# Performance work log

Measured on AMD Instinct MI355X. Metric: run time of the kernel, lower is better.

The kernel has to match this reference:

```python
import jax, jax.numpy as jnp
import numpy as np

B, L, V, D, C, R = 8, 2048, 32000, 512, 64, 64
NBLK = 2           # n_layers - 1
H = 2 * D          # stem hidden dim
STD = 0.02


def _ln(x, w, b):
    m = x.mean(-1, keepdims=True)
    v = ((x - m) ** 2).mean(-1, keepdims=True)
    return (x - m) / jnp.sqrt(v + 1e-5) * w + b


def setup_inputs() -> dict:
    key = jax.random.key(0)
    ks = jax.random.split(key, 16)
    n = lambda k, shp: jax.random.normal(k, shp, dtype=jnp.float32) * STD
    return {
        "token_ids": jax.random.randint(ks[0], (B, L), 0, V),
        "tok_emb": n(ks[1], (V, D)),
        "pos_emb": n(ks[2], (L, D)),
        "stem_ln_w": jnp.ones((NBLK, D), jnp.float32),
        "stem_ln_b": jnp.zeros((NBLK, D), jnp.float32),
        "stem_w1": n(ks[3], (NBLK, D, H)),
        "stem_b1": jnp.zeros((NBLK, H), jnp.float32),
        "stem_w2": n(ks[4], (NBLK, H, D)),
        "stem_b2": jnp.zeros((NBLK, D), jnp.float32),
        "role_ln_w": jnp.ones((D,), jnp.float32),
        "role_ln_b": jnp.zeros((D,), jnp.float32),
        "Wa": n(ks[5], (D, R)),
        "Wb": n(ks[6], (D, R)),
        "Wc": n(ks[7], (D, R)),
        "class_a": n(ks[8], (C, R)),
        "class_b": n(ks[9], (C, R)),
        "class_c": n(ks[10], (C, R)),
        "query_ln_w": jnp.ones((D,), jnp.float32),
        "query_ln_b": jnp.zeros((D,), jnp.float32),
        "Wq": n(ks[11], (D, C)),
        "bq": jnp.zeros((C,), jnp.float32),
    }


def reference(token_ids, tok_emb, pos_emb, stem_ln_w, stem_ln_b, stem_w1,
              stem_b1, stem_w2, stem_b2, role_ln_w, role_ln_b, Wa, Wb, Wc,
              class_a, class_b, class_c, query_ln_w, query_ln_b, Wq, bq):
    seq_len = token_ids.shape[1]
    x = tok_emb[token_ids] + pos_emb[:seq_len][None, :, :]  # [B,L,D]
    for i in range(NBLK):
        h = _ln(x, stem_ln_w[i], stem_ln_b[i])
        h = jax.nn.gelu(h @ stem_w1[i] + stem_b1[i], approximate=False)
        x = x + h @ stem_w2[i] + stem_b2[i]
    prefix = _ln(x[:, :-1], role_ln_w, role_ln_b)  # [B,L-1,D]
    a = jnp.tanh(prefix @ Wa)
    b = jnp.tanh(prefix @ Wb)
    c = jnp.tanh(prefix @ Wc)
    ua = jnp.einsum('blr,cr->blc', a, class_a)  # [B,L-1,C]
    ub = jnp.einsum('blr,cr->blc', b, class_b)
    uc = jnp.einsum('blr,cr->blc', c, class_c)
    # exact ordered-triplet sum  sum_{i<j<k} ua_i * ub_j * uc_k  via exclusive cumsums
    prefA = jnp.cumsum(ua, axis=1) - ua            # sum_{i<j} ua_i
    t = ub * prefA
    prefT = jnp.cumsum(t, axis=1) - t              # sum_{j<k} ub_j * prefA_j
    s = (uc * prefT).sum(axis=1)                   # [B,C]
    Lp = max(seq_len - 1, 1)
    denom = max(Lp * (Lp - 1) * (Lp - 2) / 6.0, 1.0)
    q = _ln(x[:, -1], query_ln_w, query_ln_b)
    return s / denom + q @ Wq + bq
```

## Files before the change

kernel.cpp:

```cpp
#include <hip/hip_runtime.h>

#define NROWS 16384
#define LSEQ  2048
#define NB    8

typedef short v8s __attribute__((ext_vector_type(8)));
typedef float v4f __attribute__((ext_vector_type(4)));

__device__ __forceinline__ unsigned short f2bf(float f) {
    unsigned int u = __float_as_uint(f);
    return (unsigned short)((u + 0x7fffu + ((u >> 16) & 1u)) >> 16);
}
__device__ __forceinline__ float bf2f(unsigned short u) {
    return __uint_as_float(((unsigned int)u) << 16);
}

__device__ __forceinline__ void glds16(const void* g, void* l) {
    __builtin_amdgcn_global_load_lds(
        (__attribute__((address_space(1))) void*)g,
        (__attribute__((address_space(3))) void*)l,
        16, 0, 0);
}

__device__ __forceinline__ float fast_gelu(float v) {
    float z = fabsf(v) * 0.70710678118654752f;
    float t = __builtin_amdgcn_rcpf(1.0f + 0.3275911f * z);
    float poly = t * (0.254829592f + t * (-0.284496736f + t * (1.421413741f +
                 t * (-1.453152027f + t * 1.061405429f))));
    float erfz = 1.0f - poly * __expf(-z * z);
    float er = copysignf(erfz, v);
    return 0.5f * v * (1.0f + er);
}
__device__ __forceinline__ float fast_tanh(float y) {
    float e = __expf(2.0f * y);
    return (e - 1.0f) * __builtin_amdgcn_rcpf(e + 1.0f);
}

__device__ __forceinline__ long swizzled_row(int b, int wave) {
    int T = (b & 7) + (((b >> 3) & 15) << 3);
    int chunk = b >> 7;
    return (long)T * 128 + chunk * 4 + wave;
}

__global__ __launch_bounds__(256) void setup_kernel(
        const int* __restrict__ ids,
        const float* __restrict__ tok, const float* __restrict__ pos,
        const float* __restrict__ g0, const float* __restrict__ b0,
        unsigned short* __restrict__ x, unsigned short* __restrict__ hl,
        const float* __restrict__ w1, const float* __restrict__ w2,
        const float* __restrict__ wa, const float* __restrict__ wb, const float* __restrict__ wc,
        const float* __restrict__ ca, const float* __restrict__ cb, const float* __restrict__ cc,
        unsigned short* __restrict__ w1T, unsigned short* __restrict__ w2T,
        unsigned short* __restrict__ wabcT, unsigned short* __restrict__ clsb) {
    int blk = blockIdx.x;
    int t = threadIdx.x;
    if (blk < 4096) {
        int wave = t >> 6, lane = t & 63;
        long row = swizzled_row(blk, wave);
        int l = (int)(row & (LSEQ - 1));
        int id = ids[row];
        int d = lane * 8;
        float4 t0 = *(const float4*)(tok + (size_t)id * 512 + d);
        float4 t1 = *(const float4*)(tok + (size_t)id * 512 + d + 4);
        float4 p0 = *(const float4*)(pos + (size_t)l * 512 + d);
        float4 p1 = *(const float4*)(pos + (size_t)l * 512 + d + 4);
        float a[8] = {t0.x + p0.x, t0.y + p0.y, t0.z + p0.z, t0.w + p0.w,
                      t1.x + p1.x, t1.y + p1.y, t1.z + p1.z, t1.w + p1.w};
        unsigned int xp[4];
        #pragma unroll
        for (int i = 0; i < 4; ++i)
            xp[i] = (unsigned int)f2bf(a[2 * i]) | ((unsigned int)f2bf(a[2 * i + 1]) << 16);
        *(uint4*)(x + row * 512 + d) = *(uint4*)xp;
        float s = 0.f, s2 = 0.f;
        #pragma unroll
        for (int i = 0; i < 8; ++i) { s += a[i]; s2 += a[i] * a[i]; }
        #pragma unroll
        for (int o = 32; o > 0; o >>= 1) { s += __shfl_down(s, o); s2 += __shfl_down(s2, o); }
        s = __shfl(s, 0); s2 = __shfl(s2, 0);
        float m = s * (1.0f / 512.0f);
        float rinv = 1.0f / sqrtf(s2 * (1.0f / 512.0f) - m * m + 1e-5f);
        float4 ga = *(const float4*)(g0 + d), gb = *(const float4*)(g0 + d + 4);
        float4 ba = *(const float4*)(b0 + d), bb2 = *(const float4*)(b0 + d + 4);
        float gg[8] = {ga.x, ga.y, ga.z, ga.w, gb.x, gb.y, gb.z, gb.w};
        float bb[8] = {ba.x, ba.y, ba.z, ba.w, bb2.x, bb2.y, bb2.z, bb2.w};
        unsigned int hp[4];
        #pragma unroll
        for (int i = 0; i < 4; ++i) {
            unsigned short lo = f2bf((a[2 * i]     - m) * rinv * gg[2 * i]     + bb[2 * i]);
            unsigned short hi = f2bf((a[2 * i + 1] - m) * rinv * gg[2 * i + 1] + bb[2 * i + 1]);
            hp[i] = (unsigned int)lo | ((unsigned int)hi << 16);
        }
        *(uint4*)(hl + row * 512 + d) = *(uint4*)hp;
    } else if (blk < 6240) {
        int id = blk - 4096;
        int tx = t & 31, ty = t >> 5;
        const float* in; unsigned short* out; int R, C, bx, by, ldo;
        if (id < 1024) {
            int l = id >> 9, r = id & 511;
            in = w1 + l * 524288; out = w1T + l * 524288;
            R = 512; C = 1024; bx = r & 31; by = r >> 5; ldo = 512;
        } else if (id < 2048) {
            int l = (id - 1024) >> 9, r = (id - 1024) & 511;
            in = w2 + l * 524288; out = w2T + l * 524288;
            R = 1024; C = 512; bx = r & 15; by = r >> 4; ldo = 1024;
        } else {
            int g = (id - 2048) >> 5, r = (id - 2048) & 31;
            in = (g == 0) ? wa : (g == 1) ? wb : wc;
            out = wabcT + g * 32768;
            R = 512; C = 64; bx = r & 1; by = r >> 1; ldo = 512;
        }
        __shared__ unsigned short tile[32][33];
        int c0 = bx * 32, r0 = by * 32;
        for (int i = ty; i < 32; i += 8) {
            int r = r0 + i, c = c0 + tx;
            tile[i][tx] = (r < R && c < C) ? f2bf(in[(size_t)r * C + c]) : (unsigned short)0;
        }
        __syncthreads();
        for (int i = ty; i < 32; i += 8) {
            int c = c0 + i, r = r0 + tx;
            if (r < R && c < C) out[(size_t)c * ldo + r] = tile[tx][i];
        }
    } else {
        int g = blk - 6240;
        const float* src = (g == 0) ? ca : (g == 1) ? cb : cc;
        unsigned short* dst = clsb + g * 4096;
        for (int i = t; i < 4096; i += 256) dst[i] = f2bf(src[i]);
    }
}

__global__ __launch_bounds__(256) void ln_kernel(const unsigned short* __restrict__ x,
        const float* __restrict__ g, const float* __restrict__ b,
        unsigned short* __restrict__ out) {
    int wave = threadIdx.x >> 6, lane = threadIdx.x & 63;
    long row = swizzled_row(blockIdx.x, wave);
    int d = lane * 8;
    uint4 xp = *(const uint4*)(x + row * 512 + d);
    const unsigned int* xw = (const unsigned int*)&xp;
    float a[8];
    #pragma unroll
    for (int i = 0; i < 4; ++i) {
        a[2 * i]     = bf2f((unsigned short)(xw[i] & 0xffff));
        a[2 * i + 1] = bf2f((unsigned short)(xw[i] >> 16));
    }
    float s = 0.f, s2 = 0.f;
    #pragma unroll
    for (int i = 0; i < 8; ++i) { s += a[i]; s2 += a[i] * a[i]; }
    #pragma unroll
    for (int o = 32; o > 0; o >>= 1) { s += __shfl_down(s, o); s2 += __shfl_down(s2, o); }
    s = __shfl(s, 0); s2 = __shfl(s2, 0);
    float m = s * (1.0f / 512.0f);
    float rinv = 1.0f / sqrtf(s2 * (1.0f / 512.0f) - m * m + 1e-5f);
    float4 g0 = *(const float4*)(g + d), g1 = *(const float4*)(g + d + 4);
    float4 b0 = *(const float4*)(b + d), b1 = *(const float4*)(b + d + 4);
    float gg[8] = {g0.x, g0.y, g0.z, g0.w, g1.x, g1.y, g1.z, g1.w};
    float bb[8] = {b0.x, b0.y, b0.z, b0.w, b1.x, b1.y, b1.z, b1.w};
    unsigned int hp[4];
    #pragma unroll
    for (int i = 0; i < 4; ++i) {
        unsigned short lo = f2bf((a[2 * i]     - m) * rinv * gg[2 * i]     + bb[2 * i]);
        unsigned short hi = f2bf((a[2 * i + 1] - m) * rinv * gg[2 * i + 1] + bb[2 * i + 1]);
        hp[i] = (unsigned int)lo | ((unsigned int)hi << 16);
    }
    *(uint4*)(out + row * 512 + d) = *(uint4*)hp;
}

#define EPI_GELU_BF16  0
#define EPI_RES_BF16   1

template <int EPI, int TN>
__global__ __launch_bounds__(256) void gemm_db(
        const unsigned short* __restrict__ A, int lda,
        const unsigned short* __restrict__ BT, int ldb,
        const float* __restrict__ bias,
        const unsigned short* __restrict__ xres,
        unsigned short* __restrict__ Cout, int ldc, int K) {
    constexpr int NJ = TN / 32;
    constexpr int BCH = TN / 64;
    constexpr int NL = 2 + BCH;
    __shared__ unsigned short As[3][128 * 32] __attribute__((aligned(16)));
    __shared__ unsigned short Bs[3][TN * 32] __attribute__((aligned(16)));
    const int t = threadIdx.x;
    const int lane = t & 63, wave = t >> 6;
    const int quad = lane >> 4, l16 = lane & 15;
    const int wm = (wave >> 1) * 64, wn = (wave & 1) * (TN / 2);
    const long tileM = (long)blockIdx.x * 128, tileN = (long)blockIdx.y * TN;

    const int lr = lane >> 2, lc = (lane & 3) * 8;
    const unsigned short* gA0 = A + (tileM + wave * 32 + lr) * (size_t)lda + lc;
    const unsigned short* gA1 = gA0 + 16 * (size_t)lda;
    const unsigned short* gB0 = BT + (tileN + wave * (BCH * 16) + lr) * (size_t)ldb + lc;
    const unsigned short* gB1 = gB0 + 16 * (size_t)ldb;

    v4f acc[4][NJ] = {};

    auto stage = [&](unsigned short* ab, unsigned short* bb) {
        glds16(gA0, ab + wave * 1024);
        glds16(gA1, ab + wave * 1024 + 512);
        glds16(gB0, bb + wave * (BCH * 512));
        if constexpr (BCH == 2) glds16(gB1, bb + wave * 1024 + 512);
        gA0 += 32; gA1 += 32; gB0 += 32;
        if constexpr (BCH == 2) gB1 += 32;
    };

    unsigned short *a0 = As[0], *a1 = As[1], *a2 = As[2];
    unsigned short *b0 = Bs[0], *b1 = Bs[1], *b2 = Bs[2];

    stage(a0, b0);
    stage(a1, b1);

    const int nk = K >> 5;
    for (int kk = 0; kk < nk; ++kk) {
        if (kk + 2 < nk) {
            stage(a2, b2);
            asm volatile("s_waitcnt vmcnt(%0)" :: "i"(2 * NL) : "memory");
        } else if (kk + 1 < nk) {
            asm volatile("s_waitcnt vmcnt(%0)" :: "i"(NL) : "memory");
        } else {
            asm volatile("s_waitcnt vmcnt(0)" ::: "memory");
        }
        asm volatile("s_barrier" ::: "memory");
        v8s af[4], bfr[NJ];
        #pragma unroll
        for (int i = 0; i < 4; ++i)
            af[i] = *(const v8s*)(a0 + (wm + i * 16 + l16) * 32 + quad * 8);
        #pragma unroll
        for (int j = 0; j < NJ; ++j)
            bfr[j] = *(const v8s*)(b0 + (wn + j * 16 + l16) * 32 + quad * 8);
        #pragma unroll
        for (int i = 0; i < 4; ++i)
            #pragma unroll
            for (int j = 0; j < NJ; ++j)
                acc[i][j] = __builtin_amdgcn_mfma_f32_16x16x32_bf16(bfr[j], af[i], acc[i][j], 0, 0, 0);
        if (kk + 1 < nk)
            asm volatile("s_barrier" ::: "memory");
        unsigned short* ta = a0; a0 = a1; a1 = a2; a2 = ta;
        unsigned short* tb = b0; b0 = b1; b1 = b2; b2 = tb;
    }

    #pragma unroll
    for (int i = 0; i < 4; ++i) {
        long m = tileM + wm + i * 16 + l16;
        #pragma unroll
        for (int j = 0; j < NJ; ++j) {
            long n0 = tileN + wn + j * 16 + quad * 4;
            float4 bi = *(const float4*)&bias[n0];
            const float* bip = (const float*)&bi;
            unsigned short pk[4];
            if (EPI == EPI_GELU_BF16) {
                #pragma unroll
                for (int r = 0; r < 4; ++r)
                    pk[r] = f2bf(fast_gelu(acc[i][j][r] + bip[r]));
            } else {
                ushort4 xr4 = *(const ushort4*)&xres[m * ldc + n0];
                const unsigned short* xp = (const unsigned short*)&xr4;
                #pragma unroll
                for (int r = 0; r < 4; ++r)
                    pk[r] = f2bf(acc[i][j][r] + bip[r] + bf2f(xp[r]));
            }
            *(ushort4*)&Cout[m * ldc + n0] = *(ushort4*)pk;
        }
    }
}

__global__ __launch_bounds__(256) void tanh_class_kernel(
        const unsigned short* __restrict__ A,
        const unsigned short* __restrict__ WT,
        const unsigned short* __restrict__ cls,
        unsigned short* __restrict__ uu) {
    __shared__ unsigned short As[128][40] __attribute__((aligned(16)));
    __shared__ unsigned short Bs[64][40] __attribute__((aligned(16)));
    __shared__ unsigned short P[128 * 72] __attribute__((aligned(16)));
    const int t = threadIdx.x;
    const int lane = t & 63, wave = t >> 6;
    const int quad = lane >> 4, l16 = lane & 15;
    const int wm = (wave >> 1) * 64, wn = (wave & 1) * 32;
    const long tileM = (long)blockIdx.x * 128;
    const int g = blockIdx.y;
    const int arow = t >> 2, acol = (t & 3) * 8;

    const unsigned short* BT = WT + g * 32768;
    v8s cf[2][2];
    #pragma unroll
    for (int ks = 0; ks < 2; ++ks)
        #pragma unroll
        for (int j = 0; j < 2; ++j)
            cf[ks][j] = *(const v8s*)&cls[g * 4096 + (wn + j * 16 + l16) * 64 + ks * 32 + quad * 8];

    const unsigned short* gA0 = A + (tileM + arow) * 512 + acol;
    const unsigned short* gA1 = gA0 + 64 * 512;
    const unsigned short* gB0 = BT + arow * 512 + acol;

    v4f acc[4][2] = {};
    uint4 a0, a1, b0;
    a0 = *(const uint4*)gA0; a1 = *(const uint4*)gA1; gA0 += 32; gA1 += 32;
    b0 = *(const uint4*)gB0; gB0 += 32;
    *(uint4*)&As[arow][acol] = a0;
    *(uint4*)&As[arow + 64][acol] = a1;
    *(uint4*)&Bs[arow][acol] = b0;

    for (int kk = 0; kk < 16; ++kk) {
        __syncthreads();
        const bool more = kk < 15;
        if (more) {
            a0 = *(const uint4*)gA0; a1 = *(const uint4*)gA1; gA0 += 32; gA1 += 32;
            b0 = *(const uint4*)gB0; gB0 += 32;
        }
        v8s af[4], bfr[2];
        #pragma unroll
        for (int i = 0; i < 4; ++i) af[i] = *(const v8s*)&As[wm + i * 16 + l16][quad * 8];
        #pragma unroll
        for (int j = 0; j < 2; ++j) bfr[j] = *(const v8s*)&Bs[wn + j * 16 + l16][quad * 8];
        #pragma unroll
        for (int i = 0; i < 4; ++i)
            #pragma unroll
            for (int j = 0; j < 2; ++j)
                acc[i][j] = __builtin_amdgcn_mfma_f32_16x16x32_bf16(bfr[j], af[i], acc[i][j], 0, 0, 0);
        __syncthreads();
        if (more) {
            *(uint4*)&As[arow][acol] = a0;
            *(uint4*)&As[arow + 64][acol] = a1;
            *(uint4*)&Bs[arow][acol] = b0;
        }
    }

    #pragma unroll
    for (int i = 0; i < 4; ++i) {
        int m = wm + i * 16 + l16;
        #pragma unroll
        for (int j = 0; j < 2; ++j) {
            int n0 = wn + j * 16 + quad * 4;
            unsigned short pk[4];
            #pragma unroll
            for (int r = 0; r < 4; ++r) pk[r] = f2bf(fast_tanh(acc[i][j][r]));
            *(ushort4*)&P[m * 72 + n0] = *(ushort4*)pk;
        }
    }
    __syncthreads();

    v4f acc2[4][2] = {};
    #pragma unroll
    for (int ks = 0; ks < 2; ++ks) {
        v8s paf[4];
        #pragma unroll
        for (int i = 0; i < 4; ++i)
            paf[i] = *(const v8s*)&P[(wm + i * 16 + l16) * 72 + ks * 32 + quad * 8];
        #pragma unroll
        for (int i = 0; i < 4; ++i)
            #pragma unroll
            for (int j = 0; j < 2; ++j)
                acc2[i][j] = __builtin_amdgcn_mfma_f32_16x16x32_bf16(cf[ks][j], paf[i], acc2[i][j], 0, 0, 0);
    }

    #pragma unroll
    for (int i = 0; i < 4; ++i) {
        long m = tileM + wm + i * 16 + l16;
        #pragma unroll
        for (int j = 0; j < 2; ++j) {
            int c0 = wn + j * 16 + quad * 4;
            unsigned short pk[4];
            #pragma unroll
            for (int r = 0; r < 4; ++r) pk[r] = f2bf(acc2[i][j][r]);
            *(ushort4*)&uu[m * 192 + g * 64 + c0] = *(ushort4*)pk;
        }
    }
}

__global__ __launch_bounds__(64) void scan_part_kernel(const unsigned short* __restrict__ u,
                                                       float* __restrict__ part) {
    int b = blockIdx.x, seg = blockIdx.y;
    int c = threadIdx.x;
    int l0 = seg * 32;
    int l1 = l0 + 32; if (l1 > 2047) l1 = 2047;
    float sA = 0.f, sB = 0.f, sC = 0.f, T = 0.f, M = 0.f, U = 0.f;
    const unsigned short* base = u + ((size_t)b * LSEQ + l0) * 192 + c;
    for (int l = l0; l < l1; ++l) {
        float ua = bf2f(base[0]), ub = bf2f(base[64]), uc = bf2f(base[128]);
        base += 192;
        U += uc * T;
        M += uc * sB;
        T += ub * sA;
        sA += ua; sB += ub; sC += uc;
    }
    float* p = part + ((size_t)(b * 64 + seg)) * 384 + c;
    p[0] = sA; p[64] = sB; p[128] = sC; p[192] = T; p[256] = M; p[320] = U;
}

__global__ __launch_bounds__(64) void combine_final_kernel(const float* __restrict__ part,
        const unsigned short* __restrict__ x,
        const float* __restrict__ qw, const float* __restrict__ qb,
        const float* __restrict__ Wq, const float* __restrict__ bq,
        float* __restrict__ out, float inv_denom) {
    int b = blockIdx.x;
    int c = threadIdx.x;
    const float* p = part + (size_t)b * 64 * 384 + c;
    float A = p[0], B = p[64], Tt = p[192], Mt = p[256], Ut = p[320];
    for (int seg = 1; seg < 64; ++seg) {
        const float* q2 = p + seg * 384;
        float a2 = q2[0], b2 = q2[64], c2 = q2[128], t2 = q2[192], m2 = q2[256], u2 = q2[320];
        float Un = Ut + u2 + c2 * Tt + A * m2;
        float Tn = Tt + t2 + A * b2;
        float Mn = Mt + m2 + B * c2;
        A += a2; B += b2;
        Ut = Un; Tt = Tn; Mt = Mn;
    }
    __shared__ float q[512];
    __shared__ float mv[2];
    const unsigned short* xr = x + ((size_t)b * LSEQ + (LSEQ - 1)) * 512;
    float s1 = 0.f, s2 = 0.f;
    for (int i = c; i < 512; i += 64) { float v = bf2f(xr[i]); q[i] = v; s1 += v; s2 += v * v; }
    #pragma unroll
    for (int o = 32; o > 0; o >>= 1) { s1 += __shfl_down(s1, o); s2 += __shfl_down(s2, o); }
    if (c == 0) {
        float m = s1 * (1.0f / 512.0f);
        float var = s2 * (1.0f / 512.0f) - m * m;
        mv[0] = m; mv[1] = 1.0f / sqrtf(var + 1e-5f);
    }
    __syncthreads();
    float m = mv[0], r = mv[1];
    for (int i = c; i < 512; i += 64) q[i] = (q[i] - m) * r * qw[i] + qb[i];
    __syncthreads();
    float acc = 0.f;
    for (int d = 0; d < 512; ++d) acc += q[d] * Wq[d * 64 + c];
    out[b * 64 + c] = Ut * inv_denom + acc + bq[c];
}

extern "C" void kernel_launch(void* const* d_in, const int* in_sizes, int n_in,
                              void* d_out, int out_size, void* d_ws, size_t ws_size,
                              hipStream_t stream) {
    const int*   token_ids   = (const int*)d_in[0];
    const float* tok_emb     = (const float*)d_in[1];
    const float* pos_emb     = (const float*)d_in[2];
    const float* stem_ln_w   = (const float*)d_in[3];
    const float* stem_ln_b   = (const float*)d_in[4];
    const float* stem_w1     = (const float*)d_in[5];
    const float* stem_b1     = (const float*)d_in[6];
    const float* stem_w2     = (const float*)d_in[7];
    const float* stem_b2     = (const float*)d_in[8];
    const float* role_ln_w   = (const float*)d_in[9];
    const float* role_ln_b   = (const float*)d_in[10];
    const float* Wa          = (const float*)d_in[11];
    const float* Wb          = (const float*)d_in[12];
    const float* Wc          = (const float*)d_in[13];
    const float* class_a     = (const float*)d_in[14];
    const float* class_b     = (const float*)d_in[15];
    const float* class_c     = (const float*)d_in[16];
    const float* query_ln_w  = (const float*)d_in[17];
    const float* query_ln_b  = (const float*)d_in[18];
    const float* Wq          = (const float*)d_in[19];
    const float* bq          = (const float*)d_in[20];
    float* out = (float*)d_out;

    char* wsb = (char*)d_ws;
    unsigned short* x    = (unsigned short*)(wsb);
    unsigned short* hl   = (unsigned short*)(wsb + 16777216);
    unsigned short* Hb   = (unsigned short*)(wsb + 33554432);
    unsigned short* uu   = (unsigned short*)(wsb + 67108864);
    float* part          = (float*)(wsb + 73400320);
    unsigned short* w1T  = (unsigned short*)(wsb + 74188800);
    unsigned short* w2T  = (unsigned short*)(wsb + 76285952);
    unsigned short* wabcT= (unsigned short*)(wsb + 78383104);
    unsigned short* clsb = (unsigned short*)(wsb + 78579712);

    setup_kernel<<<6243, 256, 0, stream>>>(token_ids, tok_emb, pos_emb,
        stem_ln_w, stem_ln_b, x, hl,
        stem_w1, stem_w2, Wa, Wb, Wc, class_a, class_b, class_c,
        w1T, w2T, wabcT, clsb);

    for (int i = 0; i < 2; ++i) {
        if (i > 0)
            ln_kernel<<<NROWS / 4, 256, 0, stream>>>(x, stem_ln_w + 512, stem_ln_b + 512, hl);
        gemm_db<EPI_GELU_BF16, 128><<<dim3(128, 8), 256, 0, stream>>>(
            hl, 512, w1T + i * 524288, 512, stem_b1 + i * 1024, nullptr, Hb, 1024, 512);
        gemm_db<EPI_RES_BF16, 64><<<dim3(128, 8), 256, 0, stream>>>(
            Hb, 1024, w2T + i * 524288, 1024, stem_b2 + i * 512, x, x, 512, 1024);
    }

    ln_kernel<<<NROWS / 4, 256, 0, stream>>>(x, role_ln_w, role_ln_b, hl);

    tanh_class_kernel<<<dim3(128, 3), 256, 0, stream>>>(hl, wabcT, clsb, uu);

    scan_part_kernel<<<dim3(NB, 64), 64, 0, stream>>>(uu, part);

    float inv_denom = (float)(6.0 / (2047.0 * 2046.0 * 2045.0));
    combine_final_kernel<<<NB, 64, 0, stream>>>(part, x, query_ln_w, query_ln_b,
                                                Wq, bq, out, inv_denom);
}
```

Baseline: 340.4 us.

## Swizzle LDS tiles in stem GEMMs and drop to double buffering

Applies an XOR swizzle to the 16-byte chunk index when global_load_lds fills the A/B tiles, and uses the same swizzle on the fragment reads, to cut LDS bank conflicts on MFMA operand loads. It also shrinks the pipeline from triple to double buffering, which lowers LDS use per block and may raise occupancy. The tradeoff is less load latency hidden ahead of the MFMAs, since only one stage is prefetched.

```diff
diff --git a/kernel.cpp b/kernel.cpp
--- a/kernel.cpp
+++ b/kernel.cpp
@@ -20,6 +20,10 @@
         (__attribute__((address_space(1))) void*)g,
         (__attribute__((address_space(3))) void*)l,
         16, 0, 0);
+}
+
+__device__ __forceinline__ int swz(int c) {
+    return c ^ ((((c >> 3) & 1) << 1) | (((c >> 4) & 1) << 2) | ((c >> 5) & 1));
 }
 
 __device__ __forceinline__ float fast_gelu(float v) {
@@ -168,7 +172,7 @@
 #define EPI_RES_BF16   1
 
 template <int EPI, int TN>
-__global__ __launch_bounds__(256) void gemm_db(
+__global__ __launch_bounds__(256) void gemm_swz(
         const unsigned short* __restrict__ A, int lda,
         const unsigned short* __restrict__ BT, int ldb,
         const float* __restrict__ bias,
@@ -177,43 +181,51 @@
     constexpr int NJ = TN / 32;
     constexpr int BCH = TN / 64;
     constexpr int NL = 2 + BCH;
-    __shared__ unsigned short As[3][128 * 32] __attribute__((aligned(16)));
-    __shared__ unsigned short Bs[3][TN * 32] __attribute__((aligned(16)));
+    __shared__ unsigned short As[2][128 * 32] __attribute__((aligned(16)));
+    __shared__ unsigned short Bs[2][TN * 32] __attribute__((aligned(16)));
     const int t = threadIdx.x;
     const int lane = t & 63, wave = t >> 6;
     const int quad = lane >> 4, l16 = lane & 15;
     const int wm = (wave >> 1) * 64, wn = (wave & 1) * (TN / 2);
     const long tileM = (long)blockIdx.x * 128, tileN = (long)blockIdx.y * TN;
 
-    const int lr = lane >> 2, lc = (lane & 3) * 8;
-    const unsigned short* gA0 = A + (tileM + wave * 32 + lr) * (size_t)lda + lc;
-    const unsigned short* gA1 = gA0 + 16 * (size_t)lda;
-    const unsigned short* gB0 = BT + (tileN + wave * (BCH * 16) + lr) * (size_t)ldb + lc;
-    const unsigned short* gB1 = gB0 + 16 * (size_t)ldb;
+    const int cA0 = wave * 128 + lane;
+    const int gA0c = swz(cA0), gA1c = swz(cA0 + 64);
+    const unsigned short* gA0 = A + (tileM + (gA0c >> 2)) * (size_t)lda + (gA0c & 3) * 8;
+    const unsigned short* gA1 = A + (tileM + (gA1c >> 2)) * (size_t)lda + (gA1c & 3) * 8;
+    const int cB0 = wave * (BCH * 64) + lane;
+    const int gB0c = swz(cB0);
+    const unsigned short* gB0 = BT + (tileN + (gB0c >> 2)) * (size_t)ldb + (gB0c & 3) * 8;
+    const unsigned short* gB1 = nullptr;
+    if constexpr (BCH == 2) {
+        const int gB1c = swz(cB0 + 64);
+        gB1 = BT + (tileN + (gB1c >> 2)) * (size_t)ldb + (gB1c & 3) * 8;
+    }
+
+    int aoff[4], boff[NJ];
+    #pragma unroll
+    for (int i = 0; i < 4; ++i) aoff[i] = swz((wm + i * 16 + l16) * 4 + quad) * 8;
+    #pragma unroll
+    for (int j = 0; j < NJ; ++j) boff[j] = swz((wn + j * 16 + l16) * 4 + quad) * 8;
 
     v4f acc[4][NJ] = {};
 
-    auto stage = [&](unsigned short* ab, unsigned short* bb) {
-        glds16(gA0, ab + wave * 1024);
-        glds16(gA1, ab + wave * 1024 + 512);
-        glds16(gB0, bb + wave * (BCH * 512));
-        if constexpr (BCH == 2) glds16(gB1, bb + wave * 1024 + 512);
+    auto stage = [&](int buf) {
+        glds16(gA0, &As[buf][wave * 1024]);
+        glds16(gA1, &As[buf][wave * 1024 + 512]);
+        glds16(gB0, &Bs[buf][wave * (BCH * 512)]);
+        if constexpr (BCH == 2) glds16(gB1, &Bs[buf][wave * 1024 + 512]);
         gA0 += 32; gA1 += 32; gB0 += 32;
         if constexpr (BCH == 2) gB1 += 32;
     };
 
-    unsigned short *a0 = As[0], *a1 = As[1], *a2 = As[2];
-    unsigned short *b0 = Bs[0], *b1 = Bs[1], *b2 = Bs[2];
-
-    stage(a0, b0);
-    stage(a1, b1);
+    stage(0);
 
     const int nk = K >> 5;
+    int cur = 0;
     for (int kk = 0; kk < nk; ++kk) {
-        if (kk + 2 < nk) {
-            stage(a2, b2);
-            asm volatile("s_waitcnt vmcnt(%0)" :: "i"(2 * NL) : "memory");
-        } else if (kk + 1 < nk) {
+        if (kk + 1 < nk) {
+            stage(cur ^ 1);
             asm volatile("s_waitcnt vmcnt(%0)" :: "i"(NL) : "memory");
         } else {
             asm volatile("s_waitcnt vmcnt(0)" ::: "memory");
@@ -222,10 +234,10 @@
         v8s af[4], bfr[NJ];
         #pragma unroll
         for (int i = 0; i < 4; ++i)
-            af[i] = *(const v8s*)(a0 + (wm + i * 16 + l16) * 32 + quad * 8);
+            af[i] = *(const v8s*)&As[cur][aoff[i]];
         #pragma unroll
         for (int j = 0; j < NJ; ++j)
-            bfr[j] = *(const v8s*)(b0 + (wn + j * 16 + l16) * 32 + quad * 8);
+            bfr[j] = *(const v8s*)&Bs[cur][boff[j]];
         #pragma unroll
         for (int i = 0; i < 4; ++i)
             #pragma unroll
@@ -233,8 +245,7 @@
                 acc[i][j] = __builtin_amdgcn_mfma_f32_16x16x32_bf16(bfr[j], af[i], acc[i][j], 0, 0, 0);
         if (kk + 1 < nk)
             asm volatile("s_barrier" ::: "memory");
-        unsigned short* ta = a0; a0 = a1; a1 = a2; a2 = ta;
-        unsigned short* tb = b0; b0 = b1; b1 = b2; b2 = tb;
+        cur ^= 1;
     }
 
     #pragma unroll
@@ -469,9 +480,9 @@
     for (int i = 0; i < 2; ++i) {
         if (i > 0)
             ln_kernel<<<NROWS / 4, 256, 0, stream>>>(x, stem_ln_w + 512, stem_ln_b + 512, hl);
-        gemm_db<EPI_GELU_BF16, 128><<<dim3(128, 8), 256, 0, stream>>>(
+        gemm_swz<EPI_GELU_BF16, 128><<<dim3(128, 8), 256, 0, stream>>>(
             hl, 512, w1T + i * 524288, 512, stem_b1 + i * 1024, nullptr, Hb, 1024, 512);
-        gemm_db<EPI_RES_BF16, 64><<<dim3(128, 8), 256, 0, stream>>>(
+        gemm_swz<EPI_RES_BF16, 64><<<dim3(128, 8), 256, 0, stream>>>(
             Hb, 1024, w2T + i * 524288, 1024, stem_b2 + i * 512, x, x, 512, 1024);
     }
 
```

Measured after the change: 337.1 us. No clear change (-1.0%).

## Replace stem GEMMs with 8-wave 256-row tile kernel with phased ping-pong pipeline

Applied to the files above, without the earlier changes.

Swaps the 4-wave 128-row triple-buffered GEMM for an 8-wave 256xBN tile kernel with K-step 64. Loads go straight to LDS with an XOR swizzle, and each K step is split into four MFMA phases interleaved with staged half-tile loads, barriers and s_setprio. The aim is more operand reuse per block, fewer LDS bank conflicts, and loads that overlap the MFMAs. In exchange it launches only 256 blocks, fewer than before, uses much more LDS and registers at occupancy 1, and adds many barriers.

```diff
diff --git a/kernel.cpp b/kernel.cpp
--- a/kernel.cpp
+++ b/kernel.cpp
@@ -167,95 +167,184 @@
 #define EPI_GELU_BF16  0
 #define EPI_RES_BF16   1
 
-template <int EPI, int TN>
-__global__ __launch_bounds__(256) void gemm_db(
+template <int EPI, int BN>
+__global__ __launch_bounds__(512, 1) void gemm_8p(
         const unsigned short* __restrict__ A, int lda,
         const unsigned short* __restrict__ BT, int ldb,
         const float* __restrict__ bias,
         const unsigned short* __restrict__ xres,
         unsigned short* __restrict__ Cout, int ldc, int K) {
-    constexpr int NJ = TN / 32;
-    constexpr int BCH = TN / 64;
-    constexpr int NL = 2 + BCH;
-    __shared__ unsigned short As[3][128 * 32] __attribute__((aligned(16)));
-    __shared__ unsigned short Bs[3][TN * 32] __attribute__((aligned(16)));
+    constexpr int NFC = BN / 64;
+    constexpr int FCH = NFC / 2;
+    constexpr int NLB = BN / 128;
+    constexpr int BH  = BN / 2;
+    __shared__ unsigned short Ab[2][2][128 * 64] __attribute__((aligned(16)));
+    __shared__ unsigned short Bb[2][2][BH * 64] __attribute__((aligned(16)));
     const int t = threadIdx.x;
-    const int lane = t & 63, wave = t >> 6;
+    const int lane = t & 63, w = t >> 6;
     const int quad = lane >> 4, l16 = lane & 15;
-    const int wm = (wave >> 1) * 64, wn = (wave & 1) * (TN / 2);
-    const long tileM = (long)blockIdx.x * 128, tileN = (long)blockIdx.y * TN;
-
-    const int lr = lane >> 2, lc = (lane & 3) * 8;
-    const unsigned short* gA0 = A + (tileM + wave * 32 + lr) * (size_t)lda + lc;
-    const unsigned short* gA1 = gA0 + 16 * (size_t)lda;
-    const unsigned short* gB0 = BT + (tileN + wave * (BCH * 16) + lr) * (size_t)ldb + lc;
-    const unsigned short* gB1 = gB0 + 16 * (size_t)ldb;
-
-    v4f acc[4][NJ] = {};
-
-    auto stage = [&](unsigned short* ab, unsigned short* bb) {
-        glds16(gA0, ab + wave * 1024);
-        glds16(gA1, ab + wave * 1024 + 512);
-        glds16(gB0, bb + wave * (BCH * 512));
-        if constexpr (BCH == 2) glds16(gB1, bb + wave * 1024 + 512);
-        gA0 += 32; gA1 += 32; gB0 += 32;
-        if constexpr (BCH == 2) gB1 += 32;
+    const int wmh = w >> 2;
+    const int wn  = w & 3;
+    const int bhalf = wn >> 1, bbase = (wn & 1) * (BN / 4);
+    const long tileM = (long)blockIdx.x * 256;
+    const long tileN = (long)blockIdx.y * BN;
+
+    const int rl = lane >> 3;
+    const int cl = ((lane & 7) ^ rl) * 8;
+
+    const unsigned short* pa[2][2];
+    #pragma unroll
+    for (int h = 0; h < 2; ++h)
+        #pragma unroll
+        for (int q = 0; q < 2; ++q)
+            pa[h][q] = A + (tileM + h * 128 + w * 16 + q * 8 + rl) * (size_t)lda + cl;
+    const unsigned short* pb[2][2];
+    #pragma unroll
+    for (int h = 0; h < 2; ++h) {
+        if constexpr (NLB == 2) {
+            #pragma unroll
+            for (int q = 0; q < 2; ++q)
+                pb[h][q] = BT + (tileN + h * BH + w * 16 + q * 8 + rl) * (size_t)ldb + cl;
+        } else {
+            pb[h][0] = BT + (tileN + h * BH + w * 8 + rl) * (size_t)ldb + cl;
+        }
+    }
+    int kA = 0, kB = 0;
+
+    auto stageA = [&](int buf, int h) {
+        glds16(pa[h][0] + kA, &Ab[buf][h][(w * 2 + 0) * 512]);
+        glds16(pa[h][1] + kA, &Ab[buf][h][(w * 2 + 1) * 512]);
     };
-
-    unsigned short *a0 = As[0], *a1 = As[1], *a2 = As[2];
-    unsigned short *b0 = Bs[0], *b1 = Bs[1], *b2 = Bs[2];
-
-    stage(a0, b0);
-    stage(a1, b1);
-
-    const int nk = K >> 5;
-    for (int kk = 0; kk < nk; ++kk) {
-        if (kk + 2 < nk) {
-            stage(a2, b2);
-            asm volatile("s_waitcnt vmcnt(%0)" :: "i"(2 * NL) : "memory");
-        } else if (kk + 1 < nk) {
-            asm volatile("s_waitcnt vmcnt(%0)" :: "i"(NL) : "memory");
+    auto stageB = [&](int buf, int h) {
+        if constexpr (NLB == 2) {
+            glds16(pb[h][0] + kB, &Bb[buf][h][(w * 2 + 0) * 512]);
+            glds16(pb[h][1] + kB, &Bb[buf][h][(w * 2 + 1) * 512]);
         } else {
+            glds16(pb[h][0] + kB, &Bb[buf][h][w * 512]);
+        }
+    };
+
+    const int xl = l16 & 7;
+    const int ak0 = l16 * 64 + (((quad    ) ^ xl) * 8);
+    const int ak1 = l16 * 64 + (((quad + 4) ^ xl) * 8);
+
+    stageA(0, 0); stageA(0, 1); kA = 64;
+    stageB(0, 0); stageB(0, 1); kB = 64;
+    stageB(1, 0); stageB(1, 1); kB = 128;
+
+    v4f acc[8][NFC] = {};
+    const int nt = K >> 6;
+
+    asm volatile("s_waitcnt vmcnt(%0)" :: "i"(2 * NLB) : "memory");
+    __builtin_amdgcn_s_barrier();
+
+    for (int tt = 0; tt < nt; ++tt) {
+        const int bi = tt & 1;
+        const unsigned short* Ah = &Ab[bi][wmh][0];
+        const unsigned short* Bh = &Bb[bi][bhalf][bbase * 64];
+        v8s af[4][2], bf[NFC][2];
+
+        #pragma unroll
+        for (int fr = 0; fr < 4; ++fr) {
+            af[fr][0] = *(const v8s*)(Ah + fr * 1024 + ak0);
+            af[fr][1] = *(const v8s*)(Ah + fr * 1024 + ak1);
+        }
+        #pragma unroll
+        for (int fc = 0; fc < FCH; ++fc) {
+            bf[fc][0] = *(const v8s*)(Bh + fc * 1024 + ak0);
+            bf[fc][1] = *(const v8s*)(Bh + fc * 1024 + ak1);
+        }
+        if (tt + 1 < nt) stageA(bi ^ 1, 0);
+        __builtin_amdgcn_s_barrier();
+        asm volatile("s_waitcnt lgkmcnt(0)" ::: "memory");
+        __builtin_amdgcn_s_setprio(1);
+        #pragma unroll
+        for (int fr = 0; fr < 4; ++fr)
+            #pragma unroll
+            for (int fc = 0; fc < FCH; ++fc) {
+                acc[fr][fc] = __builtin_amdgcn_mfma_f32_16x16x32_bf16(bf[fc][0], af[fr][0], acc[fr][fc], 0, 0, 0);
+                acc[fr][fc] = __builtin_amdgcn_mfma_f32_16x16x32_bf16(bf[fc][1], af[fr][1], acc[fr][fc], 0, 0, 0);
+            }
+        __builtin_amdgcn_s_setprio(0);
+        __builtin_amdgcn_s_barrier();
+
+        #pragma unroll
+        for (int fc = FCH; fc < NFC; ++fc) {
+            bf[fc][0] = *(const v8s*)(Bh + fc * 1024 + ak0);
+            bf[fc][1] = *(const v8s*)(Bh + fc * 1024 + ak1);
+        }
+        if (tt + 1 < nt) stageA(bi ^ 1, 1);
+        kA += 64;
+        __builtin_amdgcn_s_barrier();
+        asm volatile("s_waitcnt lgkmcnt(0)" ::: "memory");
+        __builtin_amdgcn_s_setprio(1);
+        #pragma unroll
+        for (int fr = 0; fr < 4; ++fr)
+            #pragma unroll
+            for (int fc = FCH; fc < NFC; ++fc) {
+                acc[fr][fc] = __builtin_amdgcn_mfma_f32_16x16x32_bf16(bf[fc][0], af[fr][0], acc[fr][fc], 0, 0, 0);
+                acc[fr][fc] = __builtin_amdgcn_mfma_f32_16x16x32_bf16(bf[fc][1], af[fr][1], acc[fr][fc], 0, 0, 0);
+            }
+        __builtin_amdgcn_s_setprio(0);
+        __builtin_amdgcn_s_barrier();
+
+        #pragma unroll
+        for (int fr = 0; fr < 4; ++fr) {
+            af[fr][0] = *(const v8s*)(Ah + (fr + 4) * 1024 + ak0);
+            af[fr][1] = *(const v8s*)(Ah + (fr + 4) * 1024 + ak1);
+        }
+        if (tt + 2 < nt) stageB(bi, 0);
+        __builtin_amdgcn_s_barrier();
+        asm volatile("s_waitcnt lgkmcnt(0)" ::: "memory");
+        __builtin_amdgcn_s_setprio(1);
+        #pragma unroll
+        for (int fr = 0; fr < 4; ++fr)
+            #pragma unroll
+            for (int fc = 0; fc < FCH; ++fc) {
+                acc[fr + 4][fc] = __builtin_amdgcn_mfma_f32_16x16x32_bf16(bf[fc][0], af[fr][0], acc[fr + 4][fc], 0, 0, 0);
+                acc[fr + 4][fc] = __builtin_amdgcn_mfma_f32_16x16x32_bf16(bf[fc][1], af[fr][1], acc[fr + 4][fc], 0, 0, 0);
+            }
+        __builtin_amdgcn_s_setprio(0);
+        __builtin_amdgcn_s_barrier();
+
+        if (tt + 2 < nt) stageB(bi, 1);
+        kB += 64;
+        if (tt + 2 < nt)
+            asm volatile("s_waitcnt vmcnt(%0)" :: "i"(2 * NLB) : "memory");
+        else if (tt + 1 < nt)
             asm volatile("s_waitcnt vmcnt(0)" ::: "memory");
-        }
-        asm volatile("s_barrier" ::: "memory");
-        v8s af[4], bfr[NJ];
-        #pragma unroll
-        for (int i = 0; i < 4; ++i)
-            af[i] = *(const v8s*)(a0 + (wm + i * 16 + l16) * 32 + quad * 8);
-        #pragma unroll
-        for (int j = 0; j < NJ; ++j)
-            bfr[j] = *(const v8s*)(b0 + (wn + j * 16 + l16) * 32 + quad * 8);
-        #pragma unroll
-        for (int i = 0; i < 4; ++i)
-            #pragma unroll
-            for (int j = 0; j < NJ; ++j)
-                acc[i][j] = __builtin_amdgcn_mfma_f32_16x16x32_bf16(bfr[j], af[i], acc[i][j], 0, 0, 0);
-        if (kk + 1 < nk)
-            asm volatile("s_barrier" ::: "memory");
-        unsigned short* ta = a0; a0 = a1; a1 = a2; a2 = ta;
-        unsigned short* tb = b0; b0 = b1; b1 = b2; b2 = tb;
-    }
-
-    #pragma unroll
-    for (int i = 0; i < 4; ++i) {
-        long m = tileM + wm + i * 16 + l16;
-        #pragma unroll
-        for (int j = 0; j < NJ; ++j) {
-            long n0 = tileN + wn + j * 16 + quad * 4;
-            float4 bi = *(const float4*)&bias[n0];
-            const float* bip = (const float*)&bi;
+        __builtin_amdgcn_s_barrier();
+        __builtin_amdgcn_s_setprio(1);
+        #pragma unroll
+        for (int fr = 0; fr < 4; ++fr)
+            #pragma unroll
+            for (int fc = FCH; fc < NFC; ++fc) {
+                acc[fr + 4][fc] = __builtin_amdgcn_mfma_f32_16x16x32_bf16(bf[fc][0], af[fr][0], acc[fr + 4][fc], 0, 0, 0);
+                acc[fr + 4][fc] = __builtin_amdgcn_mfma_f32_16x16x32_bf16(bf[fc][1], af[fr][1], acc[fr + 4][fc], 0, 0, 0);
+            }
+        __builtin_amdgcn_s_setprio(0);
+        __builtin_amdgcn_s_barrier();
+    }
+
+    #pragma unroll
+    for (int fr = 0; fr < 8; ++fr) {
+        long m = tileM + wmh * 128 + fr * 16 + l16;
+        #pragma unroll
+        for (int fc = 0; fc < NFC; ++fc) {
+            long n0 = tileN + wn * (BN / 4) + fc * 16 + quad * 4;
+            float4 bi4 = *(const float4*)&bias[n0];
+            const float* bip = (const float*)&bi4;
             unsigned short pk[4];
             if (EPI == EPI_GELU_BF16) {
                 #pragma unroll
                 for (int r = 0; r < 4; ++r)
-                    pk[r] = f2bf(fast_gelu(acc[i][j][r] + bip[r]));
+                    pk[r] = f2bf(fast_gelu(acc[fr][fc][r] + bip[r]));
             } else {
                 ushort4 xr4 = *(const ushort4*)&xres[m * ldc + n0];
                 const unsigned short* xp = (const unsigned short*)&xr4;
                 #pragma unroll
                 for (int r = 0; r < 4; ++r)
-                    pk[r] = f2bf(acc[i][j][r] + bip[r] + bf2f(xp[r]));
+                    pk[r] = f2bf(acc[fr][fc][r] + bip[r] + bf2f(xp[r]));
             }
             *(ushort4*)&Cout[m * ldc + n0] = *(ushort4*)pk;
         }
@@ -469,9 +558,9 @@
     for (int i = 0; i < 2; ++i) {
         if (i > 0)
             ln_kernel<<<NROWS / 4, 256, 0, stream>>>(x, stem_ln_w + 512, stem_ln_b + 512, hl);
-        gemm_db<EPI_GELU_BF16, 128><<<dim3(128, 8), 256, 0, stream>>>(
+        gemm_8p<EPI_GELU_BF16, 256><<<dim3(64, 4), 512, 0, stream>>>(
             hl, 512, w1T + i * 524288, 512, stem_b1 + i * 1024, nullptr, Hb, 1024, 512);
-        gemm_db<EPI_RES_BF16, 64><<<dim3(128, 8), 256, 0, stream>>>(
+        gemm_8p<EPI_RES_BF16, 128><<<dim3(64, 4), 512, 0, stream>>>(
             Hb, 1024, w2T + i * 524288, 1024, stem_b2 + i * 512, x, x, 512, 1024);
     }
 
```

After: 327.1 us. 1.04x faster.
